# Optimization experiments

Measured on AMD Instinct MI355X. Metric: run time of the kernel, lower is better.

## Reference

```python
import jax, jax.numpy as jnp
import numpy as np

B, T, S, V, H, E = 16, 128, 64, 32000, 512, 512
ATT = 512  # ATTENTION_SIZE
ATT_LAYER = 512  # ATTENTION_LAYER_SIZE


def _lstm_cell(x, c, h, Wx, Wh, b):
    # flax nn.LSTMCell math: i,f,g,o gates; c' = f*c + i*g; h' = o*tanh(c')
    g = x @ Wx + h @ Wh + b  # [B, 4H]
    i, f, gg, o = jnp.split(g, 4, axis=-1)
    c_new = jax.nn.sigmoid(f) * c + jax.nn.sigmoid(i) * jnp.tanh(gg)
    h_new = jax.nn.sigmoid(o) * jnp.tanh(c_new)
    return c_new, h_new


def setup_inputs() -> dict:
    key = jax.random.key(0)
    ks = jax.random.split(key, 20)
    def p(k, shape, fan_in):
        return jax.random.normal(k, shape, dtype=jnp.float32) / np.sqrt(fan_in)
    return {
        "tokens": jax.random.randint(ks[0], (B, T), 0, V),
        "encoder_hidden_states": jax.random.normal(ks[1], (B, S, H), dtype=jnp.float32),
        "projected_keys": jax.random.normal(ks[2], (B, S, ATT), dtype=jnp.float32),
        "attention_mask": jnp.ones((B, S), dtype=bool),
        "embedding": p(ks[3], (V, E), E),
        # layer 0: input = concat(embed, prev_attention) -> E + ATT_LAYER
        "Wx0": p(ks[4], (E + ATT_LAYER, 4 * H), E + ATT_LAYER),
        "Wh0": p(ks[5], (H, 4 * H), H),
        "b0": jnp.zeros((4 * H,), jnp.float32),
        "Wx1": p(ks[6], (H, 4 * H), H),
        "Wh1": p(ks[7], (H, 4 * H), H),
        "b1": jnp.zeros((4 * H,), jnp.float32),
        "Wq": p(ks[8], (H, ATT), H),          # MlpAttention 'query' dense (no bias)
        "w_energy": p(ks[9], (ATT,), ATT),    # MlpAttention 'energy' dense (no bias)
        "W_att": p(ks[10], (H + H, ATT_LAYER), 2 * H),  # attention_layer Dense
        "b_att": jnp.zeros((ATT_LAYER,), jnp.float32),
        "W_proj": p(ks[11], (ATT_LAYER, V), ATT_LAYER),  # projection Dense
        "b_proj": jnp.zeros((V,), jnp.float32),
    }


def reference(tokens, encoder_hidden_states, projected_keys, attention_mask,
              embedding, Wx0, Wh0, b0, Wx1, Wh1, b1, Wq, w_energy,
              W_att, b_att, W_proj, b_proj):
    # train=True, all dropout rates 0 -> dropout is identity, x comes from tokens.
    def step(carry, x_t):
        c0, h0, c1, h1, prev_att = carry
        emb = embedding[x_t]                                  # [B, E]
        lstm_in = jnp.concatenate([emb, prev_att], axis=-1)   # [B, E+ATT_LAYER]
        c0, h0 = _lstm_cell(lstm_in, c0, h0, Wx0, Wh0, b0)
        c1, h1 = _lstm_cell(h0, c1, h1, Wx1, Wh1, b1)
        h = h1                                                # [B, H]
        # Bahdanau attention
        pq = h @ Wq                                           # [B, ATT]
        energy = jnp.tanh(projected_keys + pq[:, None, :])    # [B, S, ATT]
        scores = energy @ w_energy                            # [B, S]
        scores = jnp.where(attention_mask, scores, -jnp.inf)
        scores = jax.nn.softmax(scores, axis=-1)
        context = jnp.einsum('bs,bsh->bh', scores, encoder_hidden_states)
        att = jnp.tanh(jnp.concatenate([context, h], axis=-1) @ W_att + b_att)
        logits = att @ W_proj + b_proj                        # [B, V]
        pred = jnp.argmax(logits, axis=-1).astype(jnp.uint8)
        return (c0, h0, c1, h1, att), (logits, pred, scores)

    zeros = jnp.zeros((B, H), jnp.float32)
    init = (zeros, zeros, zeros, zeros, jnp.zeros((B, ATT_LAYER), jnp.float32))
    _, (logits, preds, scores) = jax.lax.scan(step, init, tokens.T)  # scan over time
    # out_axes=1 in the original: move time to axis 1
    return (jnp.swapaxes(logits, 0, 1),
            jnp.swapaxes(preds, 0, 1),
            jnp.swapaxes(scores, 0, 1))
```

## Files before the change

### kernel.cpp

```cpp
#include <hip/hip_runtime.h>
#include <math.h>

#define BB 16
#define TT 128
#define SS 64
#define VV 32000
#define HH 512
#define G4 2048
#define LP 516

__device__ __forceinline__ float fast_tanh(float x) {
    float e = __expf(2.f * x);
    return 1.f - 2.f / (e + 1.f);
}
__device__ __forceinline__ float sigf(float x) { return 1.f / (1.f + expf(-x)); }

__global__ __launch_bounds__(256) void transpose_k(const float* __restrict__ src,
                                                   float* __restrict__ dst,
                                                   int R, int C) {
    __shared__ float tile[32][33];
    int c0 = blockIdx.x * 32, r0 = blockIdx.y * 32;
    int x = threadIdx.x, y = threadIdx.y;
    #pragma unroll
    for (int j = 0; j < 32; j += 8)
        tile[y + j][x] = src[(size_t)(r0 + y + j) * C + (c0 + x)];
    __syncthreads();
    #pragma unroll
    for (int j = 0; j < 32; j += 8)
        dst[(size_t)(c0 + y + j) * R + (r0 + x)] = tile[x][y + j];
}

template <int IS_L0>
__global__ __launch_bounds__(256) void lstm_kernel(
    int t,
    const float* __restrict__ xA,
    const float* __restrict__ hprev,
    const float* __restrict__ WaT,
    const float* __restrict__ WbT,
    const float* __restrict__ addv,
    float* __restrict__ cst,
    float* __restrict__ hout)
{
    __shared__ float xs[BB * LP];
    __shared__ float hs[BB * LP];
    __shared__ float wa[8 * 512];
    __shared__ float wb[8 * 512];
    __shared__ float red[2048];
    __shared__ float red2[128];
    const int tx  = threadIdx.x;
    const int cb  = blockIdx.x * 2;
    const int b   = tx & 15;
    const int q   = tx >> 4;
    const int kbase = (q & 7) * 64;

    #pragma unroll
    for (int rep = 0; rep < 4; ++rep) {
        const int i = tx + rep * 256;
        const int g = i >> 7;
        const int kk = (i & 127) << 2;
        const int grow = (g >> 1) * HH + cb + (g & 1);
        *(float4*)&wa[g * 512 + kk] = *(const float4*)&WaT[((size_t)grow << 9) + kk];
        *(float4*)&wb[g * 512 + kk] = *(const float4*)&WbT[((size_t)grow << 9) + kk];
    }
    {
        float v[32];
        if (IS_L0) {
            if (t > 0) {
                #pragma unroll
                for (int i = 0; i < 32; ++i) {
                    const int idx = tx + (i << 8);
                    const int r = idx >> 9, c = idx & 511;
                    v[i] = xA[((size_t)(r * TT + (t - 1)) << 9) + c];
                }
            } else {
                #pragma unroll
                for (int i = 0; i < 32; ++i) v[i] = 0.f;
            }
        } else {
            #pragma unroll
            for (int i = 0; i < 32; ++i) v[i] = xA[tx + (i << 8)];
        }
        #pragma unroll
        for (int i = 0; i < 32; ++i) {
            const int idx = tx + (i << 8);
            xs[(idx >> 9) * LP + (idx & 511)] = v[i];
        }
        #pragma unroll
        for (int i = 0; i < 32; ++i) v[i] = hprev[tx + (i << 8)];
        #pragma unroll
        for (int i = 0; i < 32; ++i) {
            const int idx = tx + (i << 8);
            hs[(idx >> 9) * LP + (idx & 511)] = v[i];
        }
    }
    __syncthreads();

    {
        const float* W  = (q < 8) ? wa : wb;
        const float* xr = (q < 8) ? &xs[b * LP] : &hs[b * LP];
        float acc[8] = {0.f,0.f,0.f,0.f,0.f,0.f,0.f,0.f};
        #pragma unroll 4
        for (int i = 0; i < 16; ++i) {
            const int k = kbase + i * 4;
            const float4 x4 = *(const float4*)&xr[k];
            #pragma unroll
            for (int g = 0; g < 8; ++g) {
                const float4 w4 = *(const float4*)&W[g * 512 + k];
                acc[g] += x4.x*w4.x + x4.y*w4.y + x4.z*w4.z + x4.w*w4.w;
            }
        }
        *(float4*)&red[q*128 + b*8]     = make_float4(acc[0],acc[1],acc[2],acc[3]);
        *(float4*)&red[q*128 + b*8 + 4] = make_float4(acc[4],acc[5],acc[6],acc[7]);
    }
    __syncthreads();
    if (tx < 128) {
        float s = 0.f;
        #pragma unroll
        for (int qq = 0; qq < 16; ++qq) s += red[qq*128 + tx];
        const int bb2 = tx >> 3, g = tx & 7;
        const int col = (g >> 1)*HH + cb + (g & 1);
        s += IS_L0 ? addv[(size_t)(bb2*TT + t) * G4 + col] : addv[col];
        red2[tx] = s;
    }
    __syncthreads();
    if (tx < 32) {
        const int bb2 = tx >> 1, cl = tx & 1;
        const float gi = red2[bb2*8 + cl],     gf = red2[bb2*8 + 2 + cl];
        const float gg = red2[bb2*8 + 4 + cl], go = red2[bb2*8 + 6 + cl];
        const int ci = (bb2 << 9) + cb + cl;
        const float c = sigf(gf) * cst[ci] + sigf(gi) * tanhf(gg);
        cst[ci] = c;
        hout[ci] = sigf(go) * tanhf(c);
    }
}

__global__ __launch_bounds__(256) void pqhw_k(
    const float* __restrict__ h1,
    const float* __restrict__ Wq,
    const float* __restrict__ Watt,
    float* __restrict__ pq_g,
    float* __restrict__ hw_g)
{
    __shared__ float h1s[512];
    __shared__ float redq[256], redh[256];
    const int b  = blockIdx.x & 15;
    const int j0 = (blockIdx.x >> 4) * 32;
    const int tx = threadIdx.x;

    {
        const float2 v = *(const float2*)&h1[(b << 9) + 2*tx];
        h1s[2*tx] = v.x; h1s[2*tx + 1] = v.y;
    }
    __syncthreads();

    const int jl = tx & 31, kp = tx >> 5;
    const int j  = j0 + jl;
    float aq = 0.f, ah = 0.f;
    #pragma unroll 8
    for (int i = 0; i < 64; ++i) {
        const int k = kp * 64 + i;
        const float hv = h1s[k];
        aq += hv * Wq[(size_t)k * HH + j];
        ah += hv * Watt[(size_t)(HH + k) * HH + j];
    }
    redq[kp*32 + jl] = aq;
    redh[kp*32 + jl] = ah;
    __syncthreads();
    if (tx < 32) {
        float s = 0.f;
        #pragma unroll
        for (int k2 = 0; k2 < 8; ++k2) s += redq[k2*32 + tx];
        pq_g[(b << 9) + j0 + tx] = s;
    } else if (tx < 64) {
        const int jl2 = tx - 32;
        float s = 0.f;
        #pragma unroll
        for (int k2 = 0; k2 < 8; ++k2) s += redh[k2*32 + jl2];
        hw_g[(b << 9) + j0 + jl2] = s;
    }
}

__global__ __launch_bounds__(256) void attn2_k(
    int t,
    const float* __restrict__ pq_g,
    const float* __restrict__ hw_g,
    const float* __restrict__ wev,
    const float* __restrict__ pk,
    const float* __restrict__ encW,
    const float* __restrict__ battv,
    float* __restrict__ att_all,
    float* __restrict__ scores)
{
    __shared__ float pqs[512], hws[512], wel[512], eng[256], prs[64];
    const int b  = blockIdx.x;
    const int tx = threadIdx.x;

    {
        const float2 v = *(const float2*)&pq_g[(b << 9) + 2*tx];
        pqs[2*tx] = v.x; pqs[2*tx + 1] = v.y;
        const float2 w = *(const float2*)&hw_g[(b << 9) + 2*tx];
        hws[2*tx] = w.x; hws[2*tx + 1] = w.y;
        const float2 u = *(const float2*)&wev[2*tx];
        wel[2*tx] = u.x; wel[2*tx + 1] = u.y;
    }
    __syncthreads();
    {
        const int s = tx >> 2, ao = tx & 3;
        const float* pkr = &pk[((size_t)(b*SS + s)) << 9];
        float p = 0.f;
        #pragma unroll 4
        for (int i = 0; i < 32; ++i) {
            const int a = ao*4 + i*16;
            const float4 kv = *(const float4*)&pkr[a];
            p += wel[a+0] * fast_tanh(kv.x + pqs[a+0]);
            p += wel[a+1] * fast_tanh(kv.y + pqs[a+1]);
            p += wel[a+2] * fast_tanh(kv.z + pqs[a+2]);
            p += wel[a+3] * fast_tanh(kv.w + pqs[a+3]);
        }
        eng[tx] = p;
    }
    __syncthreads();
    if (tx < 64) {
        const float e = eng[4*tx] + eng[4*tx+1] + eng[4*tx+2] + eng[4*tx+3];
        float m = e;
        #pragma unroll
        for (int off = 32; off >= 1; off >>= 1) m = fmaxf(m, __shfl_xor(m, off));
        const float ex = __expf(e - m);
        float sm = ex;
        #pragma unroll
        for (int off = 32; off >= 1; off >>= 1) sm += __shfl_xor(sm, off);
        const float pr = ex / sm;
        prs[tx] = pr;
        scores[((size_t)b*TT + t)*SS + tx] = pr;
    }
    __syncthreads();
    {
        float cw0 = 0.f, cw1 = 0.f;
        const float* eWb = &encW[((size_t)b * SS) << 9];
        #pragma unroll 8
        for (int s2 = 0; s2 < SS; ++s2) {
            const float w = prs[s2];
            cw0 += w * eWb[((size_t)s2 << 9) + tx];
            cw1 += w * eWb[((size_t)s2 << 9) + tx + 256];
        }
        const size_t row = ((size_t)(b*TT + t)) << 9;
        att_all[row + tx]       = tanhf(cw0 + hws[tx] + battv[tx]);
        att_all[row + tx + 256] = tanhf(cw1 + hws[tx + 256] + battv[tx + 256]);
    }
}

__global__ __launch_bounds__(256) void gemm_gather(
    const int* __restrict__ tokens, const float* __restrict__ emb,
    const float* __restrict__ Bm, const float* __restrict__ bias,
    float* __restrict__ C, int N) {
    __shared__ float As[16][68];
    __shared__ float Bs[16][132];
    __shared__ int tok[64];
    int tx = threadIdx.x;
    int r0 = blockIdx.y * 64, c0 = blockIdx.x * 128;
    if (tx < 64) tok[tx] = tokens[r0 + tx];
    __syncthreads();

    float acc[4][8];
    #pragma unroll
    for (int rr = 0; rr < 4; ++rr)
        #pragma unroll
        for (int cc = 0; cc < 8; ++cc) acc[rr][cc] = 0.f;

    int arow = tx & 63;
    int akq = tx >> 6;
    int ry = tx >> 4;
    int cx = tx & 15;
    size_t arow_base = (size_t)tok[arow] * HH;

    for (int k0 = 0; k0 < 512; k0 += 16) {
        float4 av = *(const float4*)&emb[arow_base + k0 + (akq << 2)];
        As[(akq << 2) + 0][arow] = av.x;
        As[(akq << 2) + 1][arow] = av.y;
        As[(akq << 2) + 2][arow] = av.z;
        As[(akq << 2) + 3][arow] = av.w;
        #pragma unroll
        for (int rep = 0; rep < 2; ++rep) {
            int i = tx + (rep << 8);
            int kk = i >> 5;
            int c4 = (i & 31) << 2;
            *(float4*)&Bs[kk][c4] = *(const float4*)&Bm[(size_t)(k0 + kk) * N + c0 + c4];
        }
        __syncthreads();
        #pragma unroll
        for (int kk = 0; kk < 16; ++kk) {
            float4 a4 = *(const float4*)&As[kk][ry << 2];
            float4 bA = *(const float4*)&Bs[kk][cx << 3];
            float4 bB = *(const float4*)&Bs[kk][(cx << 3) + 4];
            float ar[4] = {a4.x, a4.y, a4.z, a4.w};
            float br[8] = {bA.x, bA.y, bA.z, bA.w, bB.x, bB.y, bB.z, bB.w};
            #pragma unroll
            for (int rr = 0; rr < 4; ++rr)
                #pragma unroll
                for (int cc = 0; cc < 8; ++cc)
                    acc[rr][cc] += ar[rr] * br[cc];
        }
        __syncthreads();
    }
    #pragma unroll
    for (int rr = 0; rr < 4; ++rr) {
        int row = r0 + (ry << 2) + rr;
        #pragma unroll
        for (int cc = 0; cc < 8; ++cc) {
            int col = c0 + (cx << 3) + cc;
            C[(size_t)row * N + col] = acc[rr][cc] + bias[col];
        }
    }
}

__global__ __launch_bounds__(256) void sgemm128(
    const float* __restrict__ A, const float* __restrict__ Bm,
    const float* __restrict__ bias, float* __restrict__ C, int N) {
    __shared__ float As[16][132];
    __shared__ float Bs[16][132];
    const int tx = threadIdx.x;
    const int r0 = blockIdx.y * 128, c0 = blockIdx.x * 128;
    const int ry = tx >> 4, cx = tx & 15;

    float acc[8][8];
    #pragma unroll
    for (int rr = 0; rr < 8; ++rr)
        #pragma unroll
        for (int cc = 0; cc < 8; ++cc) acc[rr][cc] = 0.f;

    for (int k0 = 0; k0 < 512; k0 += 16) {
        #pragma unroll
        for (int rep = 0; rep < 2; ++rep) {
            const int i = tx + (rep << 8);
            const int row = i >> 2;
            const int kk = (i & 3) << 2;
            const float4 v = *(const float4*)&A[(size_t)(r0 + row) * HH + k0 + kk];
            As[kk + 0][row] = v.x; As[kk + 1][row] = v.y;
            As[kk + 2][row] = v.z; As[kk + 3][row] = v.w;
            const int kb = i >> 5;
            const int cc = (i & 31) << 2;
            *(float4*)&Bs[kb][cc] = *(const float4*)&Bm[(size_t)(k0 + kb) * N + c0 + cc];
        }
        __syncthreads();
        #pragma unroll
        for (int kk = 0; kk < 16; ++kk) {
            const float4 a0 = *(const float4*)&As[kk][ry * 8];
            const float4 a1 = *(const float4*)&As[kk][ry * 8 + 4];
            const float4 bv0 = *(const float4*)&Bs[kk][cx * 8];
            const float4 bv1 = *(const float4*)&Bs[kk][cx * 8 + 4];
            const float ar[8] = {a0.x,a0.y,a0.z,a0.w,a1.x,a1.y,a1.z,a1.w};
            const float br[8] = {bv0.x,bv0.y,bv0.z,bv0.w,bv1.x,bv1.y,bv1.z,bv1.w};
            #pragma unroll
            for (int rr = 0; rr < 8; ++rr)
                #pragma unroll
                for (int cc = 0; cc < 8; ++cc)
                    acc[rr][cc] += ar[rr] * br[cc];
        }
        __syncthreads();
    }
    float bcol[8];
    #pragma unroll
    for (int cc = 0; cc < 8; ++cc) bcol[cc] = bias[c0 + cx*8 + cc];
    #pragma unroll
    for (int rr = 0; rr < 8; ++rr) {
        const int row = r0 + ry*8 + rr;
        float4 o0 = make_float4(acc[rr][0]+bcol[0], acc[rr][1]+bcol[1],
                                acc[rr][2]+bcol[2], acc[rr][3]+bcol[3]);
        float4 o1 = make_float4(acc[rr][4]+bcol[4], acc[rr][5]+bcol[5],
                                acc[rr][6]+bcol[6], acc[rr][7]+bcol[7]);
        *(float4*)&C[(size_t)row * N + c0 + cx*8]     = o0;
        *(float4*)&C[(size_t)row * N + c0 + cx*8 + 4] = o1;
    }
}

__global__ __launch_bounds__(256) void argmax_kernel(const float* __restrict__ logits,
                                                     float* __restrict__ preds) {
    int r = blockIdx.x, tx = threadIdx.x;
    const float* row = &logits[(size_t)r * VV];
    float best = -INFINITY;
    int bi = 0x7fffffff;
    for (int i = tx; i < VV; i += 256) {
        float v = row[i];
        if (v > best) { best = v; bi = i; }
    }
    #pragma unroll
    for (int off = 1; off < 64; off <<= 1) {
        float ov = __shfl_xor(best, off);
        int oi = __shfl_xor(bi, off);
        if (ov > best || (ov == best && oi < bi)) { best = ov; bi = oi; }
    }
    __shared__ float bv[4];
    __shared__ int bidx[4];
    int w = tx >> 6;
    if ((tx & 63) == 0) { bv[w] = best; bidx[w] = bi; }
    __syncthreads();
    if (tx == 0) {
        #pragma unroll
        for (int j = 1; j < 4; ++j)
            if (bv[j] > best || (bv[j] == best && bidx[j] < bi)) { best = bv[j]; bi = bidx[j]; }
        preds[r] = (float)(bi & 255);
    }
}

extern "C" void kernel_launch(void* const* d_in, const int* in_sizes, int n_in,
                              void* d_out, int out_size, void* d_ws, size_t ws_size,
                              hipStream_t stream) {
    const int*   tokens = (const int*)d_in[0];
    const float* enc    = (const float*)d_in[1];
    const float* pk     = (const float*)d_in[2];
    const float* emb    = (const float*)d_in[4];
    const float* Wx0    = (const float*)d_in[5];
    const float* Wh0    = (const float*)d_in[6];
    const float* b0     = (const float*)d_in[7];
    const float* Wx1    = (const float*)d_in[8];
    const float* Wh1    = (const float*)d_in[9];
    const float* b1     = (const float*)d_in[10];
    const float* Wq     = (const float*)d_in[11];
    const float* we     = (const float*)d_in[12];
    const float* Watt   = (const float*)d_in[13];
    const float* batt   = (const float*)d_in[14];
    const float* Wproj  = (const float*)d_in[15];
    const float* bproj  = (const float*)d_in[16];

    float* ws = (float*)d_ws;
    float* P0    = ws;
    float* attA  = P0 + 2048 * 2048;
    float* WxT0  = attA + 2048 * 512;
    float* WhT0  = WxT0 + 2048 * 512;
    float* WxT1  = WhT0 + 2048 * 512;
    float* WhT1  = WxT1 + 2048 * 512;
    float* encW  = WhT1 + 2048 * 512;
    float* zb    = encW + 1024 * 512;
    float* st    = zb + 512;
    float* h0a = st;            float* h0b = h0a + 8192;
    float* h1a = h0b + 8192;    float* h1b = h1a + 8192;
    float* c0  = h1b + 8192;    float* c1  = c0 + 8192;
    float* pqg = c1 + 8192;     float* hwg = pqg + 8192;

    float* logits = (float*)d_out;
    float* preds  = logits + (size_t)2048 * VV;
    float* scores = preds + 2048;

    hipMemsetAsync(zb, 0, (512 + 8 * 8192) * sizeof(float), stream);

    dim3 tb(32, 8);
    transpose_k<<<dim3(2048 / 32, 512 / 32), tb, 0, stream>>>(Wx0 + 512 * 2048, WxT0, 512, 2048);
    transpose_k<<<dim3(2048 / 32, 512 / 32), tb, 0, stream>>>(Wh0, WhT0, 512, 2048);
    transpose_k<<<dim3(2048 / 32, 512 / 32), tb, 0, stream>>>(Wx1, WxT1, 512, 2048);
    transpose_k<<<dim3(2048 / 32, 512 / 32), tb, 0, stream>>>(Wh1, WhT1, 512, 2048);

    gemm_gather<<<dim3(2048 / 128, 2048 / 64), 256, 0, stream>>>(
        tokens, emb, Wx0, b0, P0, 2048);

    sgemm128<<<dim3(512 / 128, 1024 / 128), 256, 0, stream>>>(
        enc, Watt, zb, encW, 512);

    for (int t = 0; t < TT; ++t) {
        float* h0p = (t & 1) ? h0b : h0a;
        float* h0n = (t & 1) ? h0a : h0b;
        float* h1p = (t & 1) ? h1b : h1a;
        float* h1n = (t & 1) ? h1a : h1b;
        lstm_kernel<1><<<256, 256, 0, stream>>>(t, attA, h0p, WxT0, WhT0, P0, c0, h0n);
        lstm_kernel<0><<<256, 256, 0, stream>>>(t, h0n, h1p, WxT1, WhT1, b1, c1, h1n);
        pqhw_k<<<256, 256, 0, stream>>>(h1n, Wq, Watt, pqg, hwg);
        attn2_k<<<BB, 256, 0, stream>>>(t, pqg, hwg, we, pk, encW, batt,
                                        attA, scores);
    }

    sgemm128<<<dim3(VV / 128, 2048 / 128), 256, 0, stream>>>(
        attA, Wproj, bproj, logits, VV);
    argmax_kernel<<<2048, 256, 0, stream>>>(logits, preds);
}
```

Measured before the change: 5.592 ms.

## Fuse recurrent decode loop into one persistent cooperative kernel with grid barriers

Replaces the 512 per-timestep kernel launches (two LSTM layers, query projection, attention) with a single persistent cooperative kernel of 256 blocks that loops over time and uses an atomic grid barrier between phases. LSTM weight slices stay resident in LDS, Wq/Watt slices stay in registers, and cell states stay in LDS across all steps, so nothing is reloaded from global memory each step. The aim is to remove launch overhead and repeated weight loads. In exchange it needs all 256 blocks co-resident, uses heavy register and LDS pressure, and only 16 blocks do work in the attention phase while the rest wait at the barrier.

```diff
diff --git a/kernel.cpp b/kernel.cpp
--- a/kernel.cpp
+++ b/kernel.cpp
@@ -8,6 +8,7 @@
 #define HH 512
 #define G4 2048
 #define LP 516
+#define NBLK 256
 
 __device__ __forceinline__ float fast_tanh(float x) {
     float e = __expf(2.f * x);
@@ -28,225 +29,6 @@
     #pragma unroll
     for (int j = 0; j < 32; j += 8)
         dst[(size_t)(c0 + y + j) * R + (r0 + x)] = tile[x][y + j];
-}
-
-template <int IS_L0>
-__global__ __launch_bounds__(256) void lstm_kernel(
-    int t,
-    const float* __restrict__ xA,
-    const float* __restrict__ hprev,
-    const float* __restrict__ WaT,
-    const float* __restrict__ WbT,
-    const float* __restrict__ addv,
-    float* __restrict__ cst,
-    float* __restrict__ hout)
-{
-    __shared__ float xs[BB * LP];
-    __shared__ float hs[BB * LP];
-    __shared__ float wa[8 * 512];
-    __shared__ float wb[8 * 512];
-    __shared__ float red[2048];
-    __shared__ float red2[128];
-    const int tx  = threadIdx.x;
-    const int cb  = blockIdx.x * 2;
-    const int b   = tx & 15;
-    const int q   = tx >> 4;
-    const int kbase = (q & 7) * 64;
-
-    #pragma unroll
-    for (int rep = 0; rep < 4; ++rep) {
-        const int i = tx + rep * 256;
-        const int g = i >> 7;
-        const int kk = (i & 127) << 2;
-        const int grow = (g >> 1) * HH + cb + (g & 1);
-        *(float4*)&wa[g * 512 + kk] = *(const float4*)&WaT[((size_t)grow << 9) + kk];
-        *(float4*)&wb[g * 512 + kk] = *(const float4*)&WbT[((size_t)grow << 9) + kk];
-    }
-    {
-        float v[32];
-        if (IS_L0) {
-            if (t > 0) {
-                #pragma unroll
-                for (int i = 0; i < 32; ++i) {
-                    const int idx = tx + (i << 8);
-                    const int r = idx >> 9, c = idx & 511;
-                    v[i] = xA[((size_t)(r * TT + (t - 1)) << 9) + c];
-                }
-            } else {
-                #pragma unroll
-                for (int i = 0; i < 32; ++i) v[i] = 0.f;
-            }
-        } else {
-            #pragma unroll
-            for (int i = 0; i < 32; ++i) v[i] = xA[tx + (i << 8)];
-        }
-        #pragma unroll
-        for (int i = 0; i < 32; ++i) {
-            const int idx = tx + (i << 8);
-            xs[(idx >> 9) * LP + (idx & 511)] = v[i];
-        }
-        #pragma unroll
-        for (int i = 0; i < 32; ++i) v[i] = hprev[tx + (i << 8)];
-        #pragma unroll
-        for (int i = 0; i < 32; ++i) {
-            const int idx = tx + (i << 8);
-            hs[(idx >> 9) * LP + (idx & 511)] = v[i];
-        }
-    }
-    __syncthreads();
-
-    {
-        const float* W  = (q < 8) ? wa : wb;
-        const float* xr = (q < 8) ? &xs[b * LP] : &hs[b * LP];
-        float acc[8] = {0.f,0.f,0.f,0.f,0.f,0.f,0.f,0.f};
-        #pragma unroll 4
-        for (int i = 0; i < 16; ++i) {
-            const int k = kbase + i * 4;
-            const float4 x4 = *(const float4*)&xr[k];
-            #pragma unroll
-            for (int g = 0; g < 8; ++g) {
-                const float4 w4 = *(const float4*)&W[g * 512 + k];
-                acc[g] += x4.x*w4.x + x4.y*w4.y + x4.z*w4.z + x4.w*w4.w;
-            }
-        }
-        *(float4*)&red[q*128 + b*8]     = make_float4(acc[0],acc[1],acc[2],acc[3]);
-        *(float4*)&red[q*128 + b*8 + 4] = make_float4(acc[4],acc[5],acc[6],acc[7]);
-    }
-    __syncthreads();
-    if (tx < 128) {
-        float s = 0.f;
-        #pragma unroll
-        for (int qq = 0; qq < 16; ++qq) s += red[qq*128 + tx];
-        const int bb2 = tx >> 3, g = tx & 7;
-        const int col = (g >> 1)*HH + cb + (g & 1);
-        s += IS_L0 ? addv[(size_t)(bb2*TT + t) * G4 + col] : addv[col];
-        red2[tx] = s;
-    }
-    __syncthreads();
-    if (tx < 32) {
-        const int bb2 = tx >> 1, cl = tx & 1;
-        const float gi = red2[bb2*8 + cl],     gf = red2[bb2*8 + 2 + cl];
-        const float gg = red2[bb2*8 + 4 + cl], go = red2[bb2*8 + 6 + cl];
-        const int ci = (bb2 << 9) + cb + cl;
-        const float c = sigf(gf) * cst[ci] + sigf(gi) * tanhf(gg);
-        cst[ci] = c;
-        hout[ci] = sigf(go) * tanhf(c);
-    }
-}
-
-__global__ __launch_bounds__(256) void pqhw_k(
-    const float* __restrict__ h1,
-    const float* __restrict__ Wq,
-    const float* __restrict__ Watt,
-    float* __restrict__ pq_g,
-    float* __restrict__ hw_g)
-{
-    __shared__ float h1s[512];
-    __shared__ float redq[256], redh[256];
-    const int b  = blockIdx.x & 15;
-    const int j0 = (blockIdx.x >> 4) * 32;
-    const int tx = threadIdx.x;
-
-    {
-        const float2 v = *(const float2*)&h1[(b << 9) + 2*tx];
-        h1s[2*tx] = v.x; h1s[2*tx + 1] = v.y;
-    }
-    __syncthreads();
-
-    const int jl = tx & 31, kp = tx >> 5;
-    const int j  = j0 + jl;
-    float aq = 0.f, ah = 0.f;
-    #pragma unroll 8
-    for (int i = 0; i < 64; ++i) {
-        const int k = kp * 64 + i;
-        const float hv = h1s[k];
-        aq += hv * Wq[(size_t)k * HH + j];
-        ah += hv * Watt[(size_t)(HH + k) * HH + j];
-    }
-    redq[kp*32 + jl] = aq;
-    redh[kp*32 + jl] = ah;
-    __syncthreads();
-    if (tx < 32) {
-        float s = 0.f;
-        #pragma unroll
-        for (int k2 = 0; k2 < 8; ++k2) s += redq[k2*32 + tx];
-        pq_g[(b << 9) + j0 + tx] = s;
-    } else if (tx < 64) {
-        const int jl2 = tx - 32;
-        float s = 0.f;
-        #pragma unroll
-        for (int k2 = 0; k2 < 8; ++k2) s += redh[k2*32 + jl2];
-        hw_g[(b << 9) + j0 + jl2] = s;
-    }
-}
-
-__global__ __launch_bounds__(256) void attn2_k(
-    int t,
-    const float* __restrict__ pq_g,
-    const float* __restrict__ hw_g,
-    const float* __restrict__ wev,
-    const float* __restrict__ pk,
-    const float* __restrict__ encW,
-    const float* __restrict__ battv,
-    float* __restrict__ att_all,
-    float* __restrict__ scores)
-{
-    __shared__ float pqs[512], hws[512], wel[512], eng[256], prs[64];
-    const int b  = blockIdx.x;
-    const int tx = threadIdx.x;
-
-    {
-        const float2 v = *(const float2*)&pq_g[(b << 9) + 2*tx];
-        pqs[2*tx] = v.x; pqs[2*tx + 1] = v.y;
-        const float2 w = *(const float2*)&hw_g[(b << 9) + 2*tx];
-        hws[2*tx] = w.x; hws[2*tx + 1] = w.y;
-        const float2 u = *(const float2*)&wev[2*tx];
-        wel[2*tx] = u.x; wel[2*tx + 1] = u.y;
-    }
-    __syncthreads();
-    {
-        const int s = tx >> 2, ao = tx & 3;
-        const float* pkr = &pk[((size_t)(b*SS + s)) << 9];
-        float p = 0.f;
-        #pragma unroll 4
-        for (int i = 0; i < 32; ++i) {
-            const int a = ao*4 + i*16;
-            const float4 kv = *(const float4*)&pkr[a];
-            p += wel[a+0] * fast_tanh(kv.x + pqs[a+0]);
-            p += wel[a+1] * fast_tanh(kv.y + pqs[a+1]);
-            p += wel[a+2] * fast_tanh(kv.z + pqs[a+2]);
-            p += wel[a+3] * fast_tanh(kv.w + pqs[a+3]);
-        }
-        eng[tx] = p;
-    }
-    __syncthreads();
-    if (tx < 64) {
-        const float e = eng[4*tx] + eng[4*tx+1] + eng[4*tx+2] + eng[4*tx+3];
-        float m = e;
-        #pragma unroll
-        for (int off = 32; off >= 1; off >>= 1) m = fmaxf(m, __shfl_xor(m, off));
-        const float ex = __expf(e - m);
-        float sm = ex;
-        #pragma unroll
-        for (int off = 32; off >= 1; off >>= 1) sm += __shfl_xor(sm, off);
-        const float pr = ex / sm;
-        prs[tx] = pr;
-        scores[((size_t)b*TT + t)*SS + tx] = pr;
-    }
-    __syncthreads();
-    {
-        float cw0 = 0.f, cw1 = 0.f;
-        const float* eWb = &encW[((size_t)b * SS) << 9];
-        #pragma unroll 8
-        for (int s2 = 0; s2 < SS; ++s2) {
-            const float w = prs[s2];
-            cw0 += w * eWb[((size_t)s2 << 9) + tx];
-            cw1 += w * eWb[((size_t)s2 << 9) + tx + 256];
-        }
-        const size_t row = ((size_t)(b*TT + t)) << 9;
-        att_all[row + tx]       = tanhf(cw0 + hws[tx] + battv[tx]);
-        att_all[row + tx + 256] = tanhf(cw1 + hws[tx + 256] + battv[tx + 256]);
-    }
 }
 
 __global__ __launch_bounds__(256) void gemm_gather(
@@ -399,6 +181,261 @@
         for (int j = 1; j < 4; ++j)
             if (bv[j] > best || (bv[j] == best && bidx[j] < bi)) { best = bv[j]; bi = bidx[j]; }
         preds[r] = (float)(bi & 255);
+    }
+}
+
+struct DecodeArgs {
+    const float* P0;
+    const float* WxT0; const float* WhT0;
+    const float* WxT1; const float* WhT1;
+    const float* b1;
+    const float* Wq;  const float* Watt; const float* we;
+    const float* pk;  const float* encW; const float* batt;
+    float* attA;
+    float* h0a; float* h0b; float* h1a; float* h1b;
+    float* pqg; float* hwg;
+    float* scores;
+    unsigned* bar;
+};
+
+__device__ __forceinline__ void gsync(unsigned* bar, unsigned& bgen) {
+    __syncthreads();
+    ++bgen;
+    if (threadIdx.x == 0) {
+        if (__hip_atomic_fetch_add(&bar[0], 1u, __ATOMIC_ACQ_REL,
+                                   __HIP_MEMORY_SCOPE_AGENT) == NBLK - 1u) {
+            __hip_atomic_store(&bar[0], 0u, __ATOMIC_RELAXED, __HIP_MEMORY_SCOPE_AGENT);
+            __hip_atomic_store(&bar[16], bgen, __ATOMIC_RELEASE, __HIP_MEMORY_SCOPE_AGENT);
+        } else {
+            while (__hip_atomic_load(&bar[16], __ATOMIC_RELAXED,
+                                     __HIP_MEMORY_SCOPE_AGENT) < bgen)
+                __builtin_amdgcn_s_sleep(1);
+            __builtin_amdgcn_fence(__ATOMIC_ACQUIRE, "agent");
+        }
+    }
+    __syncthreads();
+}
+
+__device__ __forceinline__ void lstm_phase(
+    const int tx, const int cb, const int t, const bool xatt,
+    const float* __restrict__ xsrc, const float* __restrict__ hsrc,
+    const bool xzero, const bool hzero, const float addval,
+    const float* __restrict__ wa, const float* __restrict__ wb,
+    float* __restrict__ clds, float* __restrict__ hout,
+    float* __restrict__ xs, float* __restrict__ hs,
+    float* __restrict__ red, float* __restrict__ red2)
+{
+    #pragma unroll
+    for (int i = 0; i < 8; ++i) {
+        const int fi = tx + (i << 8);
+        const int r  = fi >> 7;
+        const int c4 = (fi & 127) << 2;
+        float4 xv = make_float4(0.f, 0.f, 0.f, 0.f);
+        if (!xzero)
+            xv = xatt ? *(const float4*)&xsrc[((size_t)(r * TT + (t - 1)) << 9) + c4]
+                      : *(const float4*)&xsrc[((size_t)r << 9) + c4];
+        *(float4*)&xs[r * LP + c4] = xv;
+        float4 hv = make_float4(0.f, 0.f, 0.f, 0.f);
+        if (!hzero) hv = *(const float4*)&hsrc[((size_t)r << 9) + c4];
+        *(float4*)&hs[r * LP + c4] = hv;
+    }
+    __syncthreads();
+    {
+        const int b = tx & 15, q = tx >> 4;
+        const int kbase = (q & 7) << 6;
+        const float* W  = (q < 8) ? wa : wb;
+        const float* xr = (q < 8) ? &xs[b * LP] : &hs[b * LP];
+        float acc[8] = {0.f,0.f,0.f,0.f,0.f,0.f,0.f,0.f};
+        #pragma unroll 4
+        for (int i = 0; i < 16; ++i) {
+            const int k = kbase + (i << 2);
+            const float4 x4 = *(const float4*)&xr[k];
+            #pragma unroll
+            for (int g = 0; g < 8; ++g) {
+                const float4 w4 = *(const float4*)&W[(g << 9) + k];
+                acc[g] += x4.x*w4.x + x4.y*w4.y + x4.z*w4.z + x4.w*w4.w;
+            }
+        }
+        *(float4*)&red[(q << 7) + (b << 3)]     = make_float4(acc[0],acc[1],acc[2],acc[3]);
+        *(float4*)&red[(q << 7) + (b << 3) + 4] = make_float4(acc[4],acc[5],acc[6],acc[7]);
+    }
+    __syncthreads();
+    if (tx < 128) {
+        float s = 0.f;
+        #pragma unroll
+        for (int qq = 0; qq < 16; ++qq) s += red[(qq << 7) + tx];
+        red2[tx] = s + addval;
+    }
+    __syncthreads();
+    if (tx < 32) {
+        const int bb2 = tx >> 1, cl = tx & 1;
+        const float gi = red2[(bb2 << 3) + cl];
+        const float gf = red2[(bb2 << 3) + 2 + cl];
+        const float gg = red2[(bb2 << 3) + 4 + cl];
+        const float go = red2[(bb2 << 3) + 6 + cl];
+        const float c = sigf(gf) * clds[(bb2 << 1) + cl] + sigf(gi) * tanhf(gg);
+        clds[(bb2 << 1) + cl] = c;
+        hout[((size_t)bb2 << 9) + cb + cl] = sigf(go) * tanhf(c);
+    }
+}
+
+__global__ void __launch_bounds__(256, 1) decode_k(DecodeArgs p) {
+    __shared__ float wa0[8 * 512], wb0[8 * 512];
+    __shared__ float wa1[8 * 512], wb1[8 * 512];
+    __shared__ float xs[BB * LP], hs[BB * LP];
+    __shared__ float red[2048];
+    __shared__ float red2[128];
+    __shared__ float c0l[32], c1l[32];
+    __shared__ float welP[512];
+
+    const int tx  = threadIdx.x;
+    const int bid = blockIdx.x;
+    const int cb  = bid << 1;
+
+    #pragma unroll
+    for (int rep = 0; rep < 4; ++rep) {
+        const int i  = tx + (rep << 8);
+        const int g  = i >> 7;
+        const int kk = (i & 127) << 2;
+        const size_t grow = (size_t)(((g >> 1) << 9) + cb + (g & 1)) << 9;
+        *(float4*)&wa0[(g << 9) + kk] = *(const float4*)&p.WxT0[grow + kk];
+        *(float4*)&wb0[(g << 9) + kk] = *(const float4*)&p.WhT0[grow + kk];
+        *(float4*)&wa1[(g << 9) + kk] = *(const float4*)&p.WxT1[grow + kk];
+        *(float4*)&wb1[(g << 9) + kk] = *(const float4*)&p.WhT1[grow + kk];
+    }
+    if (tx < 32) { c0l[tx] = 0.f; c1l[tx] = 0.f; }
+    {
+        const float2 u = *(const float2*)&p.we[tx << 1];
+        welP[tx << 1] = u.x; welP[(tx << 1) + 1] = u.y;
+    }
+
+    const int kp = tx >> 5, jl = tx & 31;
+    const int j0 = (bid >> 4) << 5;
+    const int bq = bid & 15;
+    float wqr[64], whr[64];
+    #pragma unroll
+    for (int i = 0; i < 64; ++i) {
+        const size_t k = (size_t)((kp << 6) + i);
+        wqr[i] = p.Wq[(k << 9) + j0 + jl];
+        whr[i] = p.Watt[((k + HH) << 9) + j0 + jl];
+    }
+
+    float b1v = 0.f;
+    int pcol = 0;
+    if (tx < 128) {
+        const int g = tx & 7;
+        pcol = ((g >> 1) << 9) + cb + (g & 1);
+        b1v = p.b1[pcol];
+    }
+    const float ba0 = p.batt[tx], ba1 = p.batt[tx + 256];
+
+    unsigned bgen = 0u;
+
+    for (int t = 0; t < TT; ++t) {
+        float* h0p = (t & 1) ? p.h0b : p.h0a;
+        float* h0n = (t & 1) ? p.h0a : p.h0b;
+        float* h1p = (t & 1) ? p.h1b : p.h1a;
+        float* h1n = (t & 1) ? p.h1a : p.h1b;
+
+        float a0 = 0.f;
+        if (tx < 128)
+            a0 = p.P0[(size_t)((tx >> 3) * TT + t) * G4 + pcol];
+        lstm_phase(tx, cb, t, true, p.attA, h0p, t == 0, t == 0, a0,
+                   wa0, wb0, c0l, h0n, xs, hs, red, red2);
+        gsync(p.bar, bgen);
+
+        lstm_phase(tx, cb, t, false, h0n, h1p, false, t == 0, b1v,
+                   wa1, wb1, c1l, h1n, xs, hs, red, red2);
+        gsync(p.bar, bgen);
+
+        {
+            if (tx < 128)
+                *(float4*)&xs[tx << 2] =
+                    *(const float4*)&h1n[((size_t)bq << 9) + (tx << 2)];
+            __syncthreads();
+            float aq = 0.f, ah = 0.f;
+            #pragma unroll
+            for (int i = 0; i < 64; ++i) {
+                const float hv = xs[(kp << 6) + i];
+                aq += hv * wqr[i];
+                ah += hv * whr[i];
+            }
+            red[(kp << 5) + jl]       = aq;
+            red[256 + (kp << 5) + jl] = ah;
+            __syncthreads();
+            if (tx < 32) {
+                float s = 0.f;
+                #pragma unroll
+                for (int k2 = 0; k2 < 8; ++k2) s += red[(k2 << 5) + tx];
+                p.pqg[((size_t)bq << 9) + j0 + tx] = s;
+            } else if (tx < 64) {
+                const int j2 = tx - 32;
+                float s = 0.f;
+                #pragma unroll
+                for (int k2 = 0; k2 < 8; ++k2) s += red[256 + (k2 << 5) + j2];
+                p.hwg[((size_t)bq << 9) + j0 + j2] = s;
+            }
+        }
+        gsync(p.bar, bgen);
+
+        if (bid < BB) {
+            const int b = bid;
+            float* pqs = xs;
+            float* hws = xs + 512;
+            float* eng = red;
+            float* prs = red + 256;
+            {
+                const float2 v = *(const float2*)&p.pqg[((size_t)b << 9) + (tx << 1)];
+                pqs[tx << 1] = v.x; pqs[(tx << 1) + 1] = v.y;
+                const float2 w = *(const float2*)&p.hwg[((size_t)b << 9) + (tx << 1)];
+                hws[tx << 1] = w.x; hws[(tx << 1) + 1] = w.y;
+            }
+            __syncthreads();
+            {
+                const int s = tx >> 2, ao = tx & 3;
+                const float* pkr = &p.pk[((size_t)(b * SS + s)) << 9];
+                float acc = 0.f;
+                #pragma unroll 4
+                for (int i = 0; i < 32; ++i) {
+                    const int a = (ao << 2) + (i << 4);
+                    const float4 kv = *(const float4*)&pkr[a];
+                    acc += welP[a + 0] * fast_tanh(kv.x + pqs[a + 0]);
+                    acc += welP[a + 1] * fast_tanh(kv.y + pqs[a + 1]);
+                    acc += welP[a + 2] * fast_tanh(kv.z + pqs[a + 2]);
+                    acc += welP[a + 3] * fast_tanh(kv.w + pqs[a + 3]);
+                }
+                eng[tx] = acc;
+            }
+            __syncthreads();
+            if (tx < 64) {
+                const float e = eng[4*tx] + eng[4*tx+1] + eng[4*tx+2] + eng[4*tx+3];
+                float m = e;
+                #pragma unroll
+                for (int off = 32; off >= 1; off >>= 1) m = fmaxf(m, __shfl_xor(m, off));
+                const float ex = __expf(e - m);
+                float sm = ex;
+                #pragma unroll
+                for (int off = 32; off >= 1; off >>= 1) sm += __shfl_xor(sm, off);
+                const float pr = ex / sm;
+                prs[tx] = pr;
+                p.scores[((size_t)b * TT + t) * SS + tx] = pr;
+            }
+            __syncthreads();
+            {
+                float cw0 = 0.f, cw1 = 0.f;
+                const float* eWb = &p.encW[((size_t)(b * SS)) << 9];
+                #pragma unroll 8
+                for (int s2 = 0; s2 < SS; ++s2) {
+                    const float w = prs[s2];
+                    cw0 += w * eWb[((size_t)s2 << 9) + tx];
+                    cw1 += w * eWb[((size_t)s2 << 9) + tx + 256];
+                }
+                const size_t row = ((size_t)(b * TT + t)) << 9;
+                p.attA[row + tx]       = tanhf(cw0 + hws[tx] + ba0);
+                p.attA[row + tx + 256] = tanhf(cw1 + hws[tx + 256] + ba1);
+            }
+        }
+        gsync(p.bar, bgen);
     }
 }
 
@@ -434,14 +471,14 @@
     float* st    = zb + 512;
     float* h0a = st;            float* h0b = h0a + 8192;
     float* h1a = h0b + 8192;    float* h1b = h1a + 8192;
-    float* c0  = h1b + 8192;    float* c1  = c0 + 8192;
-    float* pqg = c1 + 8192;     float* hwg = pqg + 8192;
+    float* pqg = h1b + 8192;    float* hwg = pqg + 8192;
+    unsigned* bar = (unsigned*)(zb + 480);
 
     float* logits = (float*)d_out;
     float* preds  = logits + (size_t)2048 * VV;
     float* scores = preds + 2048;
 
-    hipMemsetAsync(zb, 0, (512 + 8 * 8192) * sizeof(float), stream);
+    hipMemsetAsync(zb, 0, 512 * sizeof(float), stream);
 
     dim3 tb(32, 8);
     transpose_k<<<dim3(2048 / 32, 512 / 32), tb, 0, stream>>>(Wx0 + 512 * 2048, WxT0, 512, 2048);
@@ -455,16 +492,18 @@
     sgemm128<<<dim3(512 / 128, 1024 / 128), 256, 0, stream>>>(
         enc, Watt, zb, encW, 512);
 
-    for (int t = 0; t < TT; ++t) {
-        float* h0p = (t & 1) ? h0b : h0a;
-        float* h0n = (t & 1) ? h0a : h0b;
-        float* h1p = (t & 1) ? h1b : h1a;
-        float* h1n = (t & 1) ? h1a : h1b;
-        lstm_kernel<1><<<256, 256, 0, stream>>>(t, attA, h0p, WxT0, WhT0, P0, c0, h0n);
-        lstm_kernel<0><<<256, 256, 0, stream>>>(t, h0n, h1p, WxT1, WhT1, b1, c1, h1n);
-        pqhw_k<<<256, 256, 0, stream>>>(h1n, Wq, Watt, pqg, hwg);
-        attn2_k<<<BB, 256, 0, stream>>>(t, pqg, hwg, we, pk, encW, batt,
-                                        attA, scores);
+    DecodeArgs da;
+    da.P0 = P0; da.WxT0 = WxT0; da.WhT0 = WhT0; da.WxT1 = WxT1; da.WhT1 = WhT1;
+    da.b1 = b1; da.Wq = Wq; da.Watt = Watt; da.we = we;
+    da.pk = pk; da.encW = encW; da.batt = batt;
+    da.attA = attA;
+    da.h0a = h0a; da.h0b = h0b; da.h1a = h1a; da.h1b = h1b;
+    da.pqg = pqg; da.hwg = hwg;
+    da.scores = scores; da.bar = bar;
+    void* kargs[] = { &da };
+    if (hipLaunchCooperativeKernel((const void*)decode_k, dim3(NBLK), dim3(256),
+                                   kargs, 0, stream) != hipSuccess) {
+        decode_k<<<dim3(NBLK), dim3(256), 0, stream>>>(da);
     }
 
     sgemm128<<<dim3(VV / 128, 2048 / 128), 256, 0, stream>>>(
```

Result: slower. 9.997 ms (+78.8%).
